# Kernel tuning notes

Hardware: AMD Instinct MI355X
Metric: run time of the kernel (lower is better)

## Reference

```python
import jax, jax.numpy as jnp
import numpy as np

# Production-scale dims
B, C, T = 4, 4096, 2048      # batch, river nodes, timesteps
BS = 16                      # block_size
K = 100                      # max_delay (IRF taps)
NNZ = 1024                   # nonzero 16x16 blocks in river-network kernel
NB = C // BS                 # number of node blocks
DT = 1.0                     # dt


def setup_inputs() -> dict:
    key = jax.random.key(0)
    k1, k2, k3, k4 = jax.random.split(key, 4)
    runoff = jax.random.normal(k1, (B, C, T), jnp.float32)
    # per-entry IRF parameters (storage constants), in [0,1) -> tau in [1,20)
    params = jax.random.uniform(k2, (NNZ, BS, BS), jnp.float32)
    block_rows = jax.random.randint(k3, (NNZ,), 0, NB, jnp.int32)
    block_cols = jax.random.randint(k4, (NNZ,), 0, NB, jnp.int32)
    return {"runoff": runoff, "params": params,
            "block_rows": block_rows, "block_cols": block_cols}


def _build_kernel(params):
    # linear_storage IRF (discrete linear reservoir, cascade=1):
    #   a = exp(-dt/tau),  h[k] = (1 - a) * a**k,  k = 0..K-1 (sums ~ 1)
    tau = 1.0 + 19.0 * params                      # [NNZ, BS, BS]
    a = jnp.exp(-DT / tau)
    ks = jnp.arange(K, dtype=jnp.float32)
    h = (1.0 - a)[..., None] * jnp.power(a[..., None], ks)  # [NNZ,BS,BS,K]
    return h


def _route(runoff, params, block_rows, block_cols):
    h = _build_kernel(params)                      # [NNZ, BS(out), BS(in), K]
    # lax.conv is cross-correlation; flip taps for causal y[t]=sum_k h[k] x[t-k]
    w = h[..., ::-1].reshape(NNZ * BS, BS, K)      # grouped-conv rhs (OIH)
    xb = runoff.reshape(B, NB, BS, T)
    xg = jnp.take(xb, block_cols, axis=1)          # gather source blocks [B,NNZ,BS,T]
    xg = xg.reshape(B, NNZ * BS, T)
    # block-sparse causal conv == grouped 1D conv with left padding K-1
    y = jax.lax.conv_general_dilated(
        xg, w, window_strides=(1,), padding=[(K - 1, 0)],
        feature_group_count=NNZ, dimension_numbers=("NCH", "OIH", "NCH"))
    y = y.reshape(B, NNZ, BS, T).transpose(1, 0, 2, 3)   # [NNZ,B,BS,T]
    y = jax.ops.segment_sum(y, block_rows, num_segments=NB)  # scatter-add rows
    y = y.transpose(1, 0, 2, 3).reshape(B, C, T)
    # g.include_index_diag is False -> identity added explicitly
    return runoff + y


def reference(runoff, params, block_rows, block_cols):
    return _route(runoff, params, block_rows, block_cols)
```

## Files before the change

kernel.cpp:

```cpp
#include <hip/hip_runtime.h>

#define BB 4
#define CC 4096
#define TT 2048
#define BS 16
#define KK 100
#define NNZ 1024
#define NB (CC / BS)
#define MAXM 64
#define TC 256
#define NCH (TT / TC)
#define SSTR 260
#define HSTR 108

#define WS_CNT   0u
#define WS_PERM  1024u
#define WS_LIST  2048u
#define WS_S0    1048576u
#define S0_BYTES ((size_t)NNZ * BB * NCH * 256 * 4)
#define WS_NEED  ((size_t)WS_S0 + S0_BYTES)

template <int CTRL>
__device__ __forceinline__ float add_dpp(float acc, float src) {
    int m = __builtin_amdgcn_update_dpp(0, __builtin_bit_cast(int, src),
                                        CTRL, 0xF, 0xF, true);
    return acc + __builtin_bit_cast(float, m);
}
__device__ __forceinline__ float add_xor4(float keep, float send) {
    int m = __builtin_amdgcn_ds_swizzle(__builtin_bit_cast(int, send), 0x101F);
    return keep + __builtin_bit_cast(float, m);
}

__device__ __forceinline__ float butterfly16(const float (&v)[16], int j) {
    const bool q0 = (j & 1) != 0;
    const bool q1 = (j & 2) != 0;
    const bool q2 = (j & 4) != 0;
    const bool q3 = (j & 8) != 0;
    float u[8];
#pragma unroll
    for (int p = 0; p < 8; ++p) {
        float keep = q0 ? v[2 * p + 1] : v[2 * p];
        float send = q0 ? v[2 * p]     : v[2 * p + 1];
        u[p] = add_dpp<0xB1>(keep, send);
    }
    float w[4];
#pragma unroll
    for (int p = 0; p < 4; ++p) {
        float keep = q1 ? u[2 * p + 1] : u[2 * p];
        float send = q1 ? u[2 * p]     : u[2 * p + 1];
        w[p] = add_dpp<0x4E>(keep, send);
    }
    float z[2];
#pragma unroll
    for (int p = 0; p < 2; ++p) {
        float keep = q3 ? w[p + 2] : w[p];
        float send = q3 ? w[p]     : w[p + 2];
        z[p] = add_dpp<0x128>(keep, send);
    }
    float keep = q2 ? z[1] : z[0];
    float send = q2 ? z[0] : z[1];
    return add_xor4(keep, send);
}

__global__ __launch_bounds__(64) void lti_build_lists(
    const int* __restrict__ rows, int* __restrict__ cnt,
    int* __restrict__ list) {
    const int r = blockIdx.x;
    const int lane = threadIdx.x;
    int m = 0;
    for (int base = 0; base < NNZ; base += 64) {
        const int n = base + lane;
        const bool hit = (rows[n] == r);
        const unsigned long long mask = __ballot(hit);
        if (hit) {
            const int pos =
                m + __popcll(mask & ((1ull << lane) - 1ull));
            if (pos < MAXM) list[r * MAXM + pos] = n;
        }
        m += (int)__popcll(mask);
    }
    if (lane == 0) cnt[r] = (m < MAXM) ? m : MAXM;
}

__global__ void lti_rank(const int* __restrict__ cnt, int* __restrict__ perm) {
    __shared__ int sc[NB];
    const int r = threadIdx.x;
    sc[r] = cnt[r];
    __syncthreads();
    const int my = sc[r];
    int rank = 0;
    for (int q = 0; q < NB; ++q) {
        int cq = sc[q];
        if (cq > my || (cq == my && q < r)) ++rank;
    }
    perm[rank] = r;
}

__global__ __launch_bounds__(256) void lti_bootstrap(
    const float* __restrict__ x, const float* __restrict__ params,
    const int* __restrict__ cols, float* __restrict__ s0)
{
    const int n  = blockIdx.x;
    const int b  = blockIdx.y;
    const int ch = blockIdx.z + 1;
    const int tid = threadIdx.x;
    const int j = tid & 15;

    __shared__ __align__(16) float hx[16 * HSTR];

    const float* __restrict__ xw =
        x + ((size_t)b * CC + (size_t)cols[n] * BS) * TT + ch * TC - KK;
    {
        const int f0 = tid;
        const int row0 = f0 / 25, q0 = f0 - row0 * 25;
        if (f0 < 400) {
            *(float4*)&hx[row0 * HSTR + 4 * q0] =
                *(const float4*)(xw + (size_t)row0 * TT + 4 * q0);
        }
        const int f1 = tid + 256;
        const int row1 = f1 / 25, q1 = f1 - row1 * 25;
        if (f1 < 400) {
            *(float4*)&hx[row1 * HSTR + 4 * q1] =
                *(const float4*)(xw + (size_t)row1 * TT + 4 * q1);
        }
    }
    __syncthreads();

    const float pv  = params[n * (BS * BS) + tid];
    const float tau = 1.0f + 19.0f * pv;
    const float a   = __expf(-1.0f / tau);

    const float* __restrict__ hj = &hx[j * HSTR];
    float s = 0.0f;
#pragma unroll 5
    for (int q = 0; q < 25; ++q) {
        float4 h = *(const float4*)(hj + 4 * q);
        s = fmaf(a, s, h.x); s = fmaf(a, s, h.y);
        s = fmaf(a, s, h.z); s = fmaf(a, s, h.w);
    }
    s0[((size_t)(n * BB + b) * NCH + ch) * 256 + tid] = s;
}

__global__ __launch_bounds__(256) void lti_router(
    const float* __restrict__ x,
    const float* __restrict__ params,
    const int* __restrict__ cols,
    const int* __restrict__ cnt,
    const int* __restrict__ list,
    const int* __restrict__ perm,
    const float* __restrict__ s0,
    float* __restrict__ out)
{
    const int r   = perm[blockIdx.x];
    const int b   = blockIdx.y;
    const int ch  = blockIdx.z;
    const int t0  = ch * TC;
    const int tid = threadIdx.x;
    const int j    = tid & 15;
    const int i    = tid >> 4;
    const int lane = tid & 63;
    const int wv   = tid >> 6;

    __shared__ __align__(16) float xs[2][16 * SSTR];

    float acc[16];
#pragma unroll
    for (int p = 0; p < 16; ++p) acc[p] = 0.0f;

    const int m = cnt[r];
    const int pairs = (m + 1) >> 1;
    const size_t xbase = (size_t)b * CC * TT;

    float aA = 0.f, oA = 0.f, aB = 0.f, oB = 0.f, s0A = 0.f, s0B = 0.f;
    if (m > 0) {
        const int nA = list[r * MAXM + 0];
        const bool vB = (m > 1);
        const int nB = vB ? list[r * MAXM + 1] : nA;
        const float pvA = params[nA * (BS * BS) + tid];
        const float pvB = params[nB * (BS * BS) + tid];
        s0A = (ch == 0) ? 0.0f
            : s0[((size_t)(nA * BB + b) * NCH + ch) * 256 + tid];
        s0B = (ch == 0 || !vB) ? 0.0f
            : s0[((size_t)(nB * BB + b) * NCH + ch) * 256 + tid];
        const float* __restrict__ xA = x + xbase + (size_t)cols[nA] * BS * TT;
        const float* __restrict__ xB = x + xbase + (size_t)cols[nB] * BS * TT;
#pragma unroll
        for (int k = 0; k < 4; ++k) {
            const int row = wv + 4 * k;
            *(float4*)&xs[0][row * SSTR + lane * 4] =
                *(const float4*)(xA + (size_t)row * TT + t0 + lane * 4);
            *(float4*)&xs[1][row * SSTR + lane * 4] =
                *(const float4*)(xB + (size_t)row * TT + t0 + lane * 4);
        }
        aA = __expf(-1.0f / (1.0f + 19.0f * pvA));
        oA = 1.0f - aA;
        const float aBt = __expf(-1.0f / (1.0f + 19.0f * pvB));
        aB = vB ? aBt : 0.0f;
        oB = vB ? (1.0f - aBt) : 0.0f;
    }
    __syncthreads();

    for (int pi = 0; pi < pairs; ++pi) {
        const bool has = (pi + 1 < pairs);
        float pvNA = 0.f, pvNB = 0.f, s0NA = 0.f, s0NB = 0.f;
        bool vNB = false;
        float4 XA0, XA1, XA2, XA3, XB0, XB1, XB2, XB3;
        if (has) {
            const int ia = 2 * (pi + 1);
            const int nA = list[r * MAXM + ia];
            vNB = (ia + 1 < m);
            const int nB = vNB ? list[r * MAXM + ia + 1] : nA;
            pvNA = params[nA * (BS * BS) + tid];
            pvNB = params[nB * (BS * BS) + tid];
            s0NA = (ch == 0) ? 0.0f
                 : s0[((size_t)(nA * BB + b) * NCH + ch) * 256 + tid];
            s0NB = (ch == 0 || !vNB) ? 0.0f
                 : s0[((size_t)(nB * BB + b) * NCH + ch) * 256 + tid];
            const float* __restrict__ xA =
                x + xbase + (size_t)cols[nA] * BS * TT;
            const float* __restrict__ xB =
                x + xbase + (size_t)cols[nB] * BS * TT;
            XA0 = *(const float4*)(xA + (size_t)(wv +  0) * TT + t0 + lane * 4);
            XA1 = *(const float4*)(xA + (size_t)(wv +  4) * TT + t0 + lane * 4);
            XA2 = *(const float4*)(xA + (size_t)(wv +  8) * TT + t0 + lane * 4);
            XA3 = *(const float4*)(xA + (size_t)(wv + 12) * TT + t0 + lane * 4);
            XB0 = *(const float4*)(xB + (size_t)(wv +  0) * TT + t0 + lane * 4);
            XB1 = *(const float4*)(xB + (size_t)(wv +  4) * TT + t0 + lane * 4);
            XB2 = *(const float4*)(xB + (size_t)(wv +  8) * TT + t0 + lane * 4);
            XB3 = *(const float4*)(xB + (size_t)(wv + 12) * TT + t0 + lane * 4);
        }

        const float* __restrict__ xjA = &xs[0][j * SSTR];
        const float* __restrict__ xjB = &xs[1][j * SSTR];
        float sA = s0A, sB = s0B;
#pragma unroll
        for (int tb = 0; tb < 16; ++tb) {
            float4 A0 = *(const float4*)(xjA + tb * 16 + 0);
            float4 A1 = *(const float4*)(xjA + tb * 16 + 4);
            float4 A2 = *(const float4*)(xjA + tb * 16 + 8);
            float4 A3 = *(const float4*)(xjA + tb * 16 + 12);
            float4 B0 = *(const float4*)(xjB + tb * 16 + 0);
            float4 B1 = *(const float4*)(xjB + tb * 16 + 4);
            float4 B2 = *(const float4*)(xjB + tb * 16 + 8);
            float4 B3 = *(const float4*)(xjB + tb * 16 + 12);
            float va[16], vb[16];
            va[0]=A0.x;  va[1]=A0.y;  va[2]=A0.z;  va[3]=A0.w;
            va[4]=A1.x;  va[5]=A1.y;  va[6]=A1.z;  va[7]=A1.w;
            va[8]=A2.x;  va[9]=A2.y;  va[10]=A2.z; va[11]=A2.w;
            va[12]=A3.x; va[13]=A3.y; va[14]=A3.z; va[15]=A3.w;
            vb[0]=B0.x;  vb[1]=B0.y;  vb[2]=B0.z;  vb[3]=B0.w;
            vb[4]=B1.x;  vb[5]=B1.y;  vb[6]=B1.z;  vb[7]=B1.w;
            vb[8]=B2.x;  vb[9]=B2.y;  vb[10]=B2.z; vb[11]=B2.w;
            vb[12]=B3.x; vb[13]=B3.y; vb[14]=B3.z; vb[15]=B3.w;

            float v[16];
#pragma unroll
            for (int t = 0; t < 16; ++t) {
                sA = fmaf(aA, sA, va[t]);
                sB = fmaf(aB, sB, vb[t]);
                v[t] = fmaf(oB, sB, oA * sA);
            }
            acc[tb] += butterfly16(v, j);
        }

        if (has) {
            __syncthreads();
            *(float4*)&xs[0][(wv +  0) * SSTR + lane * 4] = XA0;
            *(float4*)&xs[0][(wv +  4) * SSTR + lane * 4] = XA1;
            *(float4*)&xs[0][(wv +  8) * SSTR + lane * 4] = XA2;
            *(float4*)&xs[0][(wv + 12) * SSTR + lane * 4] = XA3;
            *(float4*)&xs[1][(wv +  0) * SSTR + lane * 4] = XB0;
            *(float4*)&xs[1][(wv +  4) * SSTR + lane * 4] = XB1;
            *(float4*)&xs[1][(wv +  8) * SSTR + lane * 4] = XB2;
            *(float4*)&xs[1][(wv + 12) * SSTR + lane * 4] = XB3;
            aA = __expf(-1.0f / (1.0f + 19.0f * pvNA));
            oA = 1.0f - aA;
            const float aBt = __expf(-1.0f / (1.0f + 19.0f * pvNB));
            aB = vNB ? aBt : 0.0f;
            oB = vNB ? (1.0f - aBt) : 0.0f;
            s0A = s0NA; s0B = s0NB;
            __syncthreads();
        }
    }

    const size_t obase = ((size_t)b * CC + (size_t)r * BS + i) * TT + t0;
#pragma unroll
    for (int p = 0; p < 16; ++p) {
        const int t = p * 16 + j;
        out[obase + t] = x[obase + t] + acc[p];
    }
}

#define FTC 256
#define FNCH (TT / FTC)
#define FWPAD 128
#define FSSTR 388

__global__ __launch_bounds__(256) void lti_router_fb(
    const float* __restrict__ x, const float* __restrict__ params,
    const int* __restrict__ cols, const int* __restrict__ cnt,
    const int* __restrict__ list, float* __restrict__ out)
{
    const int r   = blockIdx.x;
    const int b   = blockIdx.y;
    const int t0  = blockIdx.z * FTC;
    const int tid = threadIdx.x;
    const int j   = tid & 15;
    const int i   = tid >> 4;

    __shared__ __align__(16) float xs[16 * FSSTR];

    float acc[16];
#pragma unroll
    for (int p = 0; p < 16; ++p) acc[p] = 0.0f;

    const int m = cnt[r];
    for (int bi = 0; bi < m; ++bi) {
        const int n = list[r * MAXM + bi];
        const int c = cols[n];
        const float* __restrict__ xb =
            x + ((size_t)b * CC + (size_t)c * BS) * TT;
#pragma unroll
        for (int k = 0; k < 6; ++k) {
            const int f    = tid + k * 256;
            const int row  = f / 96;
            const int col4 = f - row * 96;
            const int t    = t0 - FWPAD + col4 * 4;
            float4 v;
            if (t >= 0) v = *(const float4*)(xb + (size_t)row * TT + t);
            else        v = make_float4(0.f, 0.f, 0.f, 0.f);
            *(float4*)&xs[row * FSSTR + col4 * 4] = v;
        }
        __syncthreads();

        const float pv  = params[n * (BS * BS) + tid];
        const float tau = 1.0f + 19.0f * pv;
        const float av  = __expf(-1.0f / tau);
        const float oma = 1.0f - av;

        const float* __restrict__ xj = &xs[j * FSSTR];
        float s = 0.0f;
        if (t0 != 0) {
#pragma unroll 5
            for (int q = 0; q < 25; ++q) {
                float4 h = *(const float4*)(xj + 28 + 4 * q);
                s = fmaf(av, s, h.x); s = fmaf(av, s, h.y);
                s = fmaf(av, s, h.z); s = fmaf(av, s, h.w);
            }
        }
        const float* __restrict__ xm = xj + FWPAD;
#pragma unroll
        for (int tb = 0; tb < 16; ++tb) {
            float4 V0 = *(const float4*)(xm + tb * 16 + 0);
            float4 V1 = *(const float4*)(xm + tb * 16 + 4);
            float4 V2 = *(const float4*)(xm + tb * 16 + 8);
            float4 V3 = *(const float4*)(xm + tb * 16 + 12);
            float v[16];
            v[0]=V0.x;  v[1]=V0.y;  v[2]=V0.z;  v[3]=V0.w;
            v[4]=V1.x;  v[5]=V1.y;  v[6]=V1.z;  v[7]=V1.w;
            v[8]=V2.x;  v[9]=V2.y;  v[10]=V2.z; v[11]=V2.w;
            v[12]=V3.x; v[13]=V3.y; v[14]=V3.z; v[15]=V3.w;
#pragma unroll
            for (int t = 0; t < 16; ++t) { s = fmaf(av, s, v[t]); v[t] = oma * s; }
            acc[tb] += butterfly16(v, j);
        }
        __syncthreads();
    }

    const size_t obase = ((size_t)b * CC + (size_t)r * BS + i) * TT + t0;
#pragma unroll
    for (int p = 0; p < 16; ++p) {
        const int t = p * 16 + j;
        out[obase + t] = x[obase + t] + acc[p];
    }
}

extern "C" void kernel_launch(void* const* d_in, const int* in_sizes, int n_in,
                              void* d_out, int out_size, void* d_ws, size_t ws_size,
                              hipStream_t stream) {
    const float* runoff = (const float*)d_in[0];
    const float* params = (const float*)d_in[1];
    const int* rows = (const int*)d_in[2];
    const int* cols = (const int*)d_in[3];
    float* out = (float*)d_out;

    if (ws_size >= WS_NEED) {
        int*   cnt  = (int*)((char*)d_ws + WS_CNT);
        int*   perm = (int*)((char*)d_ws + WS_PERM);
        int*   list = (int*)((char*)d_ws + WS_LIST);
        float* s0   = (float*)((char*)d_ws + WS_S0);

        lti_build_lists<<<NB, 64, 0, stream>>>(rows, cnt, list);
        lti_rank<<<1, 256, 0, stream>>>(cnt, perm);
        dim3 bgrid(NNZ, BB, NCH - 1);
        lti_bootstrap<<<bgrid, 256, 0, stream>>>(runoff, params, cols, s0);
        dim3 rgrid(NB, BB, NCH);
        lti_router<<<rgrid, 256, 0, stream>>>(runoff, params, cols, cnt,
                                              list, perm, s0, out);
    } else {
        int* cnt  = (int*)d_ws;
        int* list = (int*)((char*)d_ws + 1024);
        lti_build_lists<<<NB, 64, 0, stream>>>(rows, cnt, list);
        dim3 grid(NB, BB, FNCH);
        lti_router_fb<<<grid, 256, 0, stream>>>(runoff, params, cols, cnt,
                                                list, out);
    }
}
```

Before: 333.8 us.

## Pre-transpose runoff into time-interleaved layout and add register-only router

Adds a transpose kernel that rewrites each 16-row runoff block so that four consecutive timesteps of all 16 rows sit together as float4 groups. A new router variant reads source blocks directly from global memory in that layout into registers and processes two nonzero blocks per iteration, with no shared-memory staging or barriers. The aim is to remove the LDS staging and synchronisation cost in the router's inner loop. In exchange it adds an extra full pass over the input, a much larger workspace (with a new tier selecting the path), and more global reads per block that now depend on the cache.

```diff
diff --git a/kernel.cpp b/kernel.cpp
--- a/kernel.cpp
+++ b/kernel.cpp
@@ -16,9 +16,12 @@
 #define WS_CNT   0u
 #define WS_PERM  1024u
 #define WS_LIST  2048u
-#define WS_S0    1048576u
+#define WS_S0    131072u
 #define S0_BYTES ((size_t)NNZ * BB * NCH * 256 * 4)
-#define WS_NEED  ((size_t)WS_S0 + S0_BYTES)
+#define WS_XT    35651584u
+#define XT_BYTES ((size_t)BB * NB * 8192 * 16)
+#define WS_NEED_MID  ((size_t)WS_S0 + S0_BYTES)
+#define WS_NEED_FULL ((size_t)WS_XT + XT_BYTES)
 
 template <int CTRL>
 __device__ __forceinline__ float add_dpp(float acc, float src) {
@@ -73,8 +76,7 @@
         const bool hit = (rows[n] == r);
         const unsigned long long mask = __ballot(hit);
         if (hit) {
-            const int pos =
-                m + __popcll(mask & ((1ull << lane) - 1ull));
+            const int pos = m + __popcll(mask & ((1ull << lane) - 1ull));
             if (pos < MAXM) list[r * MAXM + pos] = n;
         }
         m += (int)__popcll(mask);
@@ -141,7 +143,38 @@
     s0[((size_t)(n * BB + b) * NCH + ch) * 256 + tid] = s;
 }
 
-__global__ __launch_bounds__(256) void lti_router(
+__global__ __launch_bounds__(256) void lti_transpose(
+    const float* __restrict__ x, float4* __restrict__ xt4) {
+    const int c  = blockIdx.x;
+    const int b  = blockIdx.y;
+    const int t0 = blockIdx.z * 256;
+    const int tid = threadIdx.x;
+
+    __shared__ __align__(16) float xs[16 * 264];
+
+#pragma unroll
+    for (int k = 0; k < 4; ++k) {
+        const int f    = tid + k * 256;
+        const int row  = f >> 6;
+        const int col4 = f & 63;
+        *(float4*)&xs[row * 264 + col4 * 4] =
+            *(const float4*)(x + ((size_t)b * CC + (size_t)c * BS + row) * TT
+                               + t0 + col4 * 4);
+    }
+    __syncthreads();
+
+    const int j   = tid & 15;
+    const int tql = tid >> 4;
+    const size_t base = (size_t)(b * NB + c) * 8192 + (size_t)(t0 >> 2) * 16;
+#pragma unroll
+    for (int tb = 0; tb < 4; ++tb) {
+        const int tq = tb * 16 + tql;
+        float4 V = *(const float4*)&xs[j * 264 + 4 * tq];
+        xt4[base + (size_t)tq * 16 + j] = V;
+    }
+}
+
+__global__ __launch_bounds__(256) void lti_router_nt(
     const float* __restrict__ x,
     const float* __restrict__ params,
     const int* __restrict__ cols,
@@ -149,7 +182,89 @@
     const int* __restrict__ list,
     const int* __restrict__ perm,
     const float* __restrict__ s0,
+    const float4* __restrict__ xt4,
     float* __restrict__ out)
+{
+    const int r   = perm[blockIdx.x];
+    const int b   = blockIdx.y;
+    const int ch  = blockIdx.z;
+    const int t0  = ch * TC;
+    const int tid = threadIdx.x;
+    const int j   = tid & 15;
+    const int i   = tid >> 4;
+
+    float acc[16];
+#pragma unroll
+    for (int p = 0; p < 16; ++p) acc[p] = 0.0f;
+
+    const int m = cnt[r];
+    const int pairs = (m + 1) >> 1;
+
+    for (int pi = 0; pi < pairs; ++pi) {
+        const int ia = 2 * pi;
+        const int nA = list[r * MAXM + ia];
+        const bool vB = (ia + 1 < m);
+        const int nB = vB ? list[r * MAXM + ia + 1] : nA;
+        const float pvA = params[nA * (BS * BS) + tid];
+        const float pvB = params[nB * (BS * BS) + tid];
+        const float s0A = (ch == 0) ? 0.0f
+            : s0[((size_t)(nA * BB + b) * NCH + ch) * 256 + tid];
+        const float s0B = (ch == 0 || !vB) ? 0.0f
+            : s0[((size_t)(nB * BB + b) * NCH + ch) * 256 + tid];
+        const float aA  = __expf(-1.0f / (1.0f + 19.0f * pvA));
+        const float oA  = 1.0f - aA;
+        const float aBt = __expf(-1.0f / (1.0f + 19.0f * pvB));
+        const float aB  = vB ? aBt : 0.0f;
+        const float oB  = vB ? (1.0f - aBt) : 0.0f;
+
+        const float4* __restrict__ pA =
+            xt4 + (size_t)(b * NB + cols[nA]) * 8192
+                + (size_t)(t0 >> 2) * 16 + j;
+        const float4* __restrict__ pB =
+            xt4 + (size_t)(b * NB + cols[nB]) * 8192
+                + (size_t)(t0 >> 2) * 16 + j;
+
+        float sA = s0A, sB = s0B;
+#pragma unroll
+        for (int tb = 0; tb < 16; ++tb) {
+            const float4* __restrict__ qA = pA + tb * 64;
+            const float4* __restrict__ qB = pB + tb * 64;
+            float4 A0 = qA[0], A1 = qA[16], A2 = qA[32], A3 = qA[48];
+            float4 B0 = qB[0], B1 = qB[16], B2 = qB[32], B3 = qB[48];
+            float va[16], vb[16];
+            va[0]=A0.x;  va[1]=A0.y;  va[2]=A0.z;  va[3]=A0.w;
+            va[4]=A1.x;  va[5]=A1.y;  va[6]=A1.z;  va[7]=A1.w;
+            va[8]=A2.x;  va[9]=A2.y;  va[10]=A2.z; va[11]=A2.w;
+            va[12]=A3.x; va[13]=A3.y; va[14]=A3.z; va[15]=A3.w;
+            vb[0]=B0.x;  vb[1]=B0.y;  vb[2]=B0.z;  vb[3]=B0.w;
+            vb[4]=B1.x;  vb[5]=B1.y;  vb[6]=B1.z;  vb[7]=B1.w;
+            vb[8]=B2.x;  vb[9]=B2.y;  vb[10]=B2.z; vb[11]=B2.w;
+            vb[12]=B3.x; vb[13]=B3.y; vb[14]=B3.z; vb[15]=B3.w;
+
+            float v[16];
+#pragma unroll
+            for (int t = 0; t < 16; ++t) {
+                sA = fmaf(aA, sA, va[t]);
+                sB = fmaf(aB, sB, vb[t]);
+                v[t] = fmaf(oB, sB, oA * sA);
+            }
+            acc[tb] += butterfly16(v, j);
+        }
+    }
+
+    const size_t obase = ((size_t)b * CC + (size_t)r * BS + i) * TT + t0;
+#pragma unroll
+    for (int p = 0; p < 16; ++p) {
+        const int t = p * 16 + j;
+        out[obase + t] = x[obase + t] + acc[p];
+    }
+}
+
+__global__ __launch_bounds__(256) void lti_router(
+    const float* __restrict__ x, const float* __restrict__ params,
+    const int* __restrict__ cols, const int* __restrict__ cnt,
+    const int* __restrict__ list, const int* __restrict__ perm,
+    const float* __restrict__ s0, float* __restrict__ out)
 {
     const int r   = perm[blockIdx.x];
     const int b   = blockIdx.y;
@@ -384,11 +499,25 @@
     const int* cols = (const int*)d_in[3];
     float* out = (float*)d_out;
 
-    if (ws_size >= WS_NEED) {
-        int*   cnt  = (int*)((char*)d_ws + WS_CNT);
-        int*   perm = (int*)((char*)d_ws + WS_PERM);
-        int*   list = (int*)((char*)d_ws + WS_LIST);
-        float* s0   = (float*)((char*)d_ws + WS_S0);
+    int* cnt  = (int*)((char*)d_ws + WS_CNT);
+    int* perm = (int*)((char*)d_ws + WS_PERM);
+    int* list = (int*)((char*)d_ws + WS_LIST);
+
+    if (ws_size >= WS_NEED_FULL) {
+        float*  s0  = (float*)((char*)d_ws + WS_S0);
+        float4* xt4 = (float4*)((char*)d_ws + WS_XT);
+
+        lti_build_lists<<<NB, 64, 0, stream>>>(rows, cnt, list);
+        lti_rank<<<1, 256, 0, stream>>>(cnt, perm);
+        dim3 bgrid(NNZ, BB, NCH - 1);
+        lti_bootstrap<<<bgrid, 256, 0, stream>>>(runoff, params, cols, s0);
+        dim3 tgrid(NB, BB, TT / 256);
+        lti_transpose<<<tgrid, 256, 0, stream>>>(runoff, xt4);
+        dim3 rgrid(NB, BB, NCH);
+        lti_router_nt<<<rgrid, 256, 0, stream>>>(runoff, params, cols, cnt,
+                                                 list, perm, s0, xt4, out);
+    } else if (ws_size >= WS_NEED_MID) {
+        float* s0 = (float*)((char*)d_ws + WS_S0);
 
         lti_build_lists<<<NB, 64, 0, stream>>>(rows, cnt, list);
         lti_rank<<<1, 256, 0, stream>>>(cnt, perm);
@@ -398,11 +527,11 @@
         lti_router<<<rgrid, 256, 0, stream>>>(runoff, params, cols, cnt,
                                               list, perm, s0, out);
     } else {
-        int* cnt  = (int*)d_ws;
-        int* list = (int*)((char*)d_ws + 1024);
-        lti_build_lists<<<NB, 64, 0, stream>>>(rows, cnt, list);
+        int* cnt2  = (int*)d_ws;
+        int* list2 = (int*)((char*)d_ws + 1024);
+        lti_build_lists<<<NB, 64, 0, stream>>>(rows, cnt2, list2);
         dim3 grid(NB, BB, FNCH);
-        lti_router_fb<<<grid, 256, 0, stream>>>(runoff, params, cols, cnt,
-                                                list, out);
-    }
-}
+        lti_router_fb<<<grid, 256, 0, stream>>>(runoff, params, cols, cnt2,
+                                                list2, out);
+    }
+}
```

Measured after the change: 469.9 us. 1.41x slower.
